# Performance work log

Measured on AMD Instinct MI355X. Metric: run time of the kernel, lower is better.

## Reference

```python
import jax, jax.numpy as jnp
import numpy as np

D_MODEL = 1024
N_HEAD = 16
HEAD_SIZE = D_MODEL // N_HEAD


def setup_inputs() -> dict:
    key = jax.random.key(0)
    ks = jax.random.split(key, 7)
    B, T, E = 2, 2048, D_MODEL
    scale = 0.02
    return {
        "q": jax.random.normal(ks[0], (B, T, E), dtype=jnp.float32),
        "k": jax.random.normal(ks[1], (B, T, E), dtype=jnp.float32),
        "v": jax.random.normal(ks[2], (B, T, E), dtype=jnp.float32),
        "Wq": jax.random.normal(ks[3], (E, E), dtype=jnp.float32) * scale,
        "Wk": jax.random.normal(ks[4], (E, E), dtype=jnp.float32) * scale,
        "Wv": jax.random.normal(ks[5], (E, E), dtype=jnp.float32) * scale,
        "Wo": jax.random.normal(ks[6], (E, E), dtype=jnp.float32) * scale,
    }


def reference(q, k, v, Wq, Wk, Wv, Wo):
    B, T, E = q.shape
    # torch nn.Linear(bias=False): y = x @ W.T
    qh = (q @ Wq.T).reshape(B, T, N_HEAD, HEAD_SIZE).transpose(0, 2, 1, 3)  # [B,H,T,Dh]
    kh = (k @ Wk.T).reshape(B, T, N_HEAD, HEAD_SIZE).transpose(0, 2, 1, 3)
    vh = (v @ Wv.T).reshape(B, T, N_HEAD, HEAD_SIZE).transpose(0, 2, 1, 3)

    scale = 1.0 / jnp.sqrt(jnp.asarray(HEAD_SIZE, dtype=q.dtype))
    wei = jnp.einsum("bhqd,bhkd->bhqk", qh, kh) * scale  # [B,H,T,T]

    # causal mask (tril): positions j > i set to -inf
    causal = jnp.tril(jnp.ones((T, T), dtype=bool))
    wei = jnp.where(causal, wei, jnp.asarray(-jnp.inf, dtype=wei.dtype))

    attn = jax.nn.softmax(wei, axis=-1)
    out = jnp.einsum("bhqk,bhkd->bhqd", attn, vh)  # [B,H,T,Dh]
    out = out.transpose(0, 2, 1, 3).reshape(B, T, E)
    return out @ Wo.T  # dropout p=0.0 -> identity
```

## Files before the change

kernel.cpp:

```cpp
#include <hip/hip_runtime.h>
#include <hip/hip_bf16.h>
#include <cstddef>
#include <cstdint>

#define B_SZ   2
#define T_SEQ  2048
#define E_DIM  1024
#define N_HEAD 16
#define HEAD   64

typedef unsigned short u16;
typedef unsigned int u32;
using frag8 = __attribute__((ext_vector_type(8))) short;
using f32x4 = __attribute__((ext_vector_type(4))) float;

__device__ inline u16 f2bf(float x) {
    __hip_bfloat16 h = __float2bfloat16(x);
    return *reinterpret_cast<u16*>(&h);
}

__device__ inline void gl2lds16(const void* g, void* l) {
    auto gp = reinterpret_cast<const __attribute__((address_space(1))) unsigned int*>(
        reinterpret_cast<uintptr_t>(g));
    auto lp = reinterpret_cast<__attribute__((address_space(3))) unsigned int*>(
        reinterpret_cast<uintptr_t>(l));
    __builtin_amdgcn_global_load_lds(gp, lp, 16, 0, 0);
}

struct CastArgs {
    const float* src[7];
    u16* dst[7];
    int n[7];
    float scale[7];
};

__global__ __launch_bounds__(256) void cast_f32_bf16(CastArgs a) {
    const int t = blockIdx.y;
    const int i0 = (blockIdx.x * 256 + threadIdx.x) * 8;
    if (i0 >= a.n[t]) return;
    const float sc = a.scale[t];
    const float4 f0 = *(const float4*)(a.src[t] + i0);
    const float4 f1 = *(const float4*)(a.src[t] + i0 + 4);
    union { u16 s[8]; uint4 v; } r;
    r.s[0] = f2bf(f0.x * sc); r.s[1] = f2bf(f0.y * sc);
    r.s[2] = f2bf(f0.z * sc); r.s[3] = f2bf(f0.w * sc);
    r.s[4] = f2bf(f1.x * sc); r.s[5] = f2bf(f1.y * sc);
    r.s[6] = f2bf(f1.z * sc); r.s[7] = f2bf(f1.w * sc);
    *(uint4*)(a.dst[t] + i0) = r.v;
}

__device__ inline void gemm_core(const u16* __restrict__ X,
                                 const u16* __restrict__ W,
                                 void* __restrict__ Yv, int mode,
                                 int bm0, int bn0) {
    __shared__ u16 As[2][64 * 64];
    __shared__ u16 Bs[2][128 * 64];

    const int tid = threadIdx.x;
    const int w = tid >> 6;
    const int lane = tid & 63;
    const int ln = lane & 15;
    const int quad = lane >> 4;
    const int wm = (w & 1) * 32;
    const int wn = (w >> 1) * 64;

    const int l8 = lane >> 3;
    const int g = (lane & 7) ^ l8;

    const u16* Ag = X + (size_t)(bm0 + w * 16 + l8) * 1024 + g * 8;
    const u16* Bg = W + (size_t)(bn0 + w * 32 + l8) * 1024 + g * 8;
    const int al = __builtin_amdgcn_readfirstlane(w * 1024);
    const int bl = __builtin_amdgcn_readfirstlane(w * 2048);

    const f32x4 zf = {0.f, 0.f, 0.f, 0.f};
    f32x4 acc[2][4];
#pragma unroll
    for (int mi = 0; mi < 2; ++mi)
#pragma unroll
        for (int nj = 0; nj < 4; ++nj) acc[mi][nj] = zf;

    const int sw = ln & 7;

    gl2lds16(Ag, &As[0][0] + al);
    gl2lds16(Ag + 8 * 1024, &As[0][0] + al + 512);
#pragma unroll
    for (int it = 0; it < 4; ++it)
        gl2lds16(Bg + (size_t)it * 8 * 1024, &Bs[0][0] + bl + it * 512);

    for (int k0 = 0; k0 < 1024; k0 += 64) {
        const int buf = (k0 >> 6) & 1;
        __syncthreads();

        if (k0 + 64 < 1024) {
            gl2lds16(Ag + k0 + 64, &As[buf ^ 1][0] + al);
            gl2lds16(Ag + 8 * 1024 + k0 + 64, &As[buf ^ 1][0] + al + 512);
#pragma unroll
            for (int it = 0; it < 4; ++it)
                gl2lds16(Bg + (size_t)it * 8 * 1024 + k0 + 64,
                         &Bs[buf ^ 1][0] + bl + it * 512);
        }

        frag8 a[2][2], b[4][2];
#pragma unroll
        for (int kc = 0; kc < 2; ++kc) {
            const int slot = ((kc * 4 + quad) ^ sw) * 8;
#pragma unroll
            for (int mi = 0; mi < 2; ++mi)
                a[mi][kc] = *(const frag8*)(&As[buf][0] + (wm + mi * 16 + ln) * 64 + slot);
#pragma unroll
            for (int nj = 0; nj < 4; ++nj)
                b[nj][kc] = *(const frag8*)(&Bs[buf][0] + (wn + nj * 16 + ln) * 64 + slot);
        }
#pragma unroll
        for (int kc = 0; kc < 2; ++kc)
#pragma unroll
            for (int mi = 0; mi < 2; ++mi)
#pragma unroll
                for (int nj = 0; nj < 4; ++nj)
                    acc[mi][nj] = __builtin_amdgcn_mfma_f32_16x16x32_bf16(
                        a[mi][kc], b[nj][kc], acc[mi][nj], 0, 0, 0);
    }

#pragma unroll
    for (int mi = 0; mi < 2; ++mi)
#pragma unroll
        for (int nj = 0; nj < 4; ++nj)
#pragma unroll
            for (int reg = 0; reg < 4; ++reg) {
                const int m = bm0 + wm + mi * 16 + quad * 4 + reg;
                const int n = bn0 + wn + nj * 16 + ln;
                if (mode == 1) {
                    ((float*)Yv)[(size_t)m * E_DIM + n] = acc[mi][nj][reg];
                } else {
                    const int b_ = m >> 11, t_ = m & (T_SEQ - 1);
                    const int h_ = n >> 6, d_ = n & (HEAD - 1);
                    const size_t idx = (mode == 0)
                        ? (((size_t)(b_ * N_HEAD + h_)) * T_SEQ + t_) * HEAD + d_
                        : (((size_t)(b_ * N_HEAD + h_)) * HEAD + d_) * T_SEQ + t_;
                    ((u16*)Yv)[idx] = f2bf(acc[mi][nj][reg]);
                }
            }
}

struct QkvArgs {
    const u16* X[3];
    const u16* W[3];
    u16* Y[3];
};

__global__ __launch_bounds__(256, 3) void gemm_qkv(QkvArgs a) {
    const int z = blockIdx.z;
    gemm_core(a.X[z], a.W[z], a.Y[z], z == 2 ? 2 : 0,
              blockIdx.x * 64, blockIdx.y * 128);
}

__global__ __launch_bounds__(256, 3) void gemm_out(const u16* __restrict__ X,
                                                   const u16* __restrict__ W,
                                                   float* __restrict__ Y) {
    gemm_core(X, W, Y, 1, blockIdx.x * 64, blockIdx.y * 128);
}

__global__ __launch_bounds__(256, 2) void attn_mfma(const u16* __restrict__ Qh,
                                                    const u16* __restrict__ Kh,
                                                    const u16* __restrict__ Vt_g,
                                                    u16* __restrict__ Aa) {
    __shared__ u16 Ks[2][128 * 64];
    __shared__ u16 Vs[2][64 * 128];

    const int tid = threadIdx.x;
    const int w = tid >> 6;
    const int lane = tid & 63;
    const int ln = lane & 15;
    const int quad = lane >> 4;

    const int i = blockIdx.x;
    const int half = i >> 8;
    const int r_ = i & 255;
    const int bh = r_ >> 3;
    const int j = r_ & 7;
    const int qt = half ? j : (15 - j);
    const int q0 = qt * 128;
    const int qw = q0 + w * 32;

    const size_t base = (size_t)bh * T_SEQ * HEAD;
    const u16* Qb = Qh + base;
    const u16* Kb = Kh + base;
    const u16* Vtb = Vt_g + base;

    const int l8 = lane >> 3;
    const int gk = (lane & 7) ^ l8;
    const int l16 = lane >> 4;
    const int c16 = lane & 15;
    const int sls = __builtin_amdgcn_readfirstlane(w * 2048);

    frag8 qf[2][2];
#pragma unroll
    for (int qq = 0; qq < 2; ++qq)
#pragma unroll
        for (int kc = 0; kc < 2; ++kc)
            qf[qq][kc] = *(const frag8*)(Qb + (size_t)(qw + qq * 16 + ln) * HEAD +
                                         kc * 32 + quad * 8);

    const f32x4 zf = {0.f, 0.f, 0.f, 0.f};
    f32x4 o[4][2];
    float rsl[2] = {0.f, 0.f};
#pragma unroll
    for (int dt = 0; dt < 4; ++dt)
#pragma unroll
        for (int qq = 0; qq < 2; ++qq) o[dt][qq] = zf;

    const int ktiles = qt + 1;

#pragma unroll
    for (int it = 0; it < 4; ++it) {
        const int krow = w * 32 + it * 8 + l8;
        gl2lds16(Kb + (size_t)krow * HEAD + gk * 8, &Ks[0][0] + sls + it * 512);
        const int vrow = w * 16 + it * 4 + l16;
        const int gv = c16 ^ (vrow & 7);
        gl2lds16(Vtb + (size_t)vrow * T_SEQ + gv * 8, &Vs[0][0] + sls + it * 512);
    }

    const int sw = ln & 7;
    const int hsel = quad >> 1;
    const int s_lo = ((quad & 1) * 2) * 16 + ln;
    const int s_hi = s_lo + 16;

    for (int kt = 0; kt < ktiles; ++kt) {
        const int k0 = kt << 7;
        const int buf = kt & 1;
        __syncthreads();

        if (kt + 1 < ktiles) {
            const int k1 = k0 + 128;
#pragma unroll
            for (int it = 0; it < 4; ++it) {
                const int krow = w * 32 + it * 8 + l8;
                gl2lds16(Kb + (size_t)(k1 + krow) * HEAD + gk * 8,
                         &Ks[buf ^ 1][0] + sls + it * 512);
                const int vrow = w * 16 + it * 4 + l16;
                const int gv = c16 ^ (vrow & 7);
                gl2lds16(Vtb + (size_t)vrow * T_SEQ + k1 + gv * 8,
                         &Vs[buf ^ 1][0] + sls + it * 512);
            }
        }

        const bool msk = (k0 + 127 > qw);
        u32 pk[8][2][2];
#pragma unroll
        for (int kk = 0; kk < 8; ++kk) {
            f32x4 st[2] = {zf, zf};
#pragma unroll
            for (int kc = 0; kc < 2; ++kc) {
                const int slot = ((kc * 4 + quad) ^ sw) * 8;
                const frag8 kf = *(const frag8*)(&Ks[buf][0] + (kk * 16 + ln) * 64 + slot);
                st[0] = __builtin_amdgcn_mfma_f32_16x16x32_bf16(kf, qf[0][kc], st[0], 0, 0, 0);
                st[1] = __builtin_amdgcn_mfma_f32_16x16x32_bf16(kf, qf[1][kc], st[1], 0, 0, 0);
            }
#pragma unroll
            for (int qq = 0; qq < 2; ++qq) {
                float e[4];
#pragma unroll
                for (int reg = 0; reg < 4; ++reg) {
                    const int key = k0 + kk * 16 + quad * 4 + reg;
                    const int qg = qw + qq * 16 + ln;
                    float ev = __expf(st[qq][reg]);
                    if (msk) ev = (key <= qg) ? ev : 0.f;
                    e[reg] = ev;
                    rsl[qq] += ev;
                }
                pk[kk][qq][0] = ((u32)f2bf(e[1]) << 16) | f2bf(e[0]);
                pk[kk][qq][1] = ((u32)f2bf(e[3]) << 16) | f2bf(e[2]);
            }
        }

#pragma unroll
        for (int kc = 0; kc < 4; ++kc) {
            union { frag8 f; u32 d[4]; } pb[2];
#pragma unroll
            for (int qq = 0; qq < 2; ++qq) {
                const u32 a00 = __shfl(pk[kc * 2][qq][0], s_lo, 64);
                const u32 a01 = __shfl(pk[kc * 2][qq][1], s_lo, 64);
                const u32 a02 = __shfl(pk[kc * 2][qq][0], s_hi, 64);
                const u32 a03 = __shfl(pk[kc * 2][qq][1], s_hi, 64);
                const u32 a10 = __shfl(pk[kc * 2 + 1][qq][0], s_lo, 64);
                const u32 a11 = __shfl(pk[kc * 2 + 1][qq][1], s_lo, 64);
                const u32 a12 = __shfl(pk[kc * 2 + 1][qq][0], s_hi, 64);
                const u32 a13 = __shfl(pk[kc * 2 + 1][qq][1], s_hi, 64);
                pb[qq].d[0] = hsel ? a10 : a00;
                pb[qq].d[1] = hsel ? a11 : a01;
                pb[qq].d[2] = hsel ? a12 : a02;
                pb[qq].d[3] = hsel ? a13 : a03;
            }
            const int slot = ((kc * 4 + quad) ^ sw) * 8;
#pragma unroll
            for (int dt = 0; dt < 4; ++dt) {
                const frag8 vf = *(const frag8*)(&Vs[buf][0] + (dt * 16 + ln) * 128 + slot);
                o[dt][0] = __builtin_amdgcn_mfma_f32_16x16x32_bf16(vf, pb[0].f, o[dt][0], 0, 0, 0);
                o[dt][1] = __builtin_amdgcn_mfma_f32_16x16x32_bf16(vf, pb[1].f, o[dt][1], 0, 0, 0);
            }
        }
    }

#pragma unroll
    for (int qq = 0; qq < 2; ++qq) {
        rsl[qq] += __shfl_xor(rsl[qq], 16, 64);
        rsl[qq] += __shfl_xor(rsl[qq], 32, 64);
    }
    const float inv0 = 1.f / rsl[0];
    const float inv1 = 1.f / rsl[1];
    const int b_ = bh >> 4, h_ = bh & (N_HEAD - 1);
#pragma unroll
    for (int qq = 0; qq < 2; ++qq) {
        const float inv = qq ? inv1 : inv0;
        const int qg = qw + qq * 16 + ln;
        u16* rowp = Aa + ((size_t)(b_ * T_SEQ + qg)) * E_DIM + h_ * HEAD;
#pragma unroll
        for (int dt = 0; dt < 4; ++dt)
#pragma unroll
            for (int rp = 0; rp < 2; ++rp) {
                const u32 v = ((u32)f2bf(o[dt][qq][2 * rp + 1] * inv) << 16) |
                              f2bf(o[dt][qq][2 * rp] * inv);
                *(u32*)(rowp + dt * 16 + quad * 4 + rp * 2) = v;
            }
    }
}

extern "C" void kernel_launch(void* const* d_in, const int* in_sizes, int n_in,
                              void* d_out, int out_size, void* d_ws, size_t ws_size,
                              hipStream_t stream) {
    const float* q  = (const float*)d_in[0];
    const float* k  = (const float*)d_in[1];
    const float* v  = (const float*)d_in[2];
    const float* Wq = (const float*)d_in[3];
    const float* Wk = (const float*)d_in[4];
    const float* Wv = (const float*)d_in[5];
    const float* Wo = (const float*)d_in[6];

    u16* ws = (u16*)d_ws;
    const size_t M4 = (size_t)4 * 1024 * 1024;
    const size_t M1 = (size_t)1024 * 1024;
    u16* qb  = ws;
    u16* kb  = ws + M4;
    u16* vb  = ws + 2 * M4;
    u16* Wqb = ws + 3 * M4;
    u16* Wkb = ws + 3 * M4 + M1;
    u16* Wvb = ws + 3 * M4 + 2 * M1;
    u16* Wob = ws + 3 * M4 + 3 * M1;
    u16* Qh  = ws + 4 * M4;
    u16* Kh  = ws + 5 * M4;
    u16* Vht = ws + 6 * M4;
    u16* Aa  = ws + 7 * M4;

    CastArgs ca;
    ca.src[0] = q;  ca.src[1] = k;  ca.src[2] = v;
    ca.src[3] = Wq; ca.src[4] = Wk; ca.src[5] = Wv; ca.src[6] = Wo;
    ca.dst[0] = qb;  ca.dst[1] = kb;  ca.dst[2] = vb;
    ca.dst[3] = Wqb; ca.dst[4] = Wkb; ca.dst[5] = Wvb; ca.dst[6] = Wob;
    ca.n[0] = ca.n[1] = ca.n[2] = (int)M4;
    ca.n[3] = ca.n[4] = ca.n[5] = ca.n[6] = (int)M1;
    ca.scale[0] = ca.scale[1] = ca.scale[2] = 1.f;
    ca.scale[3] = 0.125f;
    ca.scale[4] = ca.scale[5] = ca.scale[6] = 1.f;
    cast_f32_bf16<<<dim3(2048, 7), 256, 0, stream>>>(ca);

    QkvArgs ga;
    ga.X[0] = qb;  ga.X[1] = kb;  ga.X[2] = vb;
    ga.W[0] = Wqb; ga.W[1] = Wkb; ga.W[2] = Wvb;
    ga.Y[0] = Qh;  ga.Y[1] = Kh;  ga.Y[2] = Vht;
    gemm_qkv<<<dim3(64, 8, 3), 256, 0, stream>>>(ga);

    attn_mfma<<<dim3(512), 256, 0, stream>>>(Qh, Kh, Vht, Aa);

    gemm_out<<<dim3(64, 8), 256, 0, stream>>>(Aa, Wob, (float*)d_out);
}
```

Measured before the change: 207.1 us.

## Split attention key tiles across two wave groups with LDS reduction

Doubles the attention block to 512 threads: the two groups of four waves share the same query rows and each handles half of every 128-key tile. Partial output accumulators and row sums are combined through LDS at the end. Wave groups whose key half lies wholly above the causal diagonal skip their work. This is meant to raise wave parallelism and shorten each wave's serial key loop, at the cost of an extra reduction, more barriers and tighter register limits from launch_bounds(512,4).

```diff
diff --git a/kernel.cpp b/kernel.cpp
--- a/kernel.cpp
+++ b/kernel.cpp
@@ -160,7 +160,7 @@
     gemm_core(X, W, Y, 1, blockIdx.x * 64, blockIdx.y * 128);
 }
 
-__global__ __launch_bounds__(256, 2) void attn_mfma(const u16* __restrict__ Qh,
+__global__ __launch_bounds__(512, 4) void attn_mfma(const u16* __restrict__ Qh,
                                                     const u16* __restrict__ Kh,
                                                     const u16* __restrict__ Vt_g,
                                                     u16* __restrict__ Aa) {
@@ -169,6 +169,8 @@
 
     const int tid = threadIdx.x;
     const int w = tid >> 6;
+    const int wq = w & 3;
+    const int wk = w >> 2;
     const int lane = tid & 63;
     const int ln = lane & 15;
     const int quad = lane >> 4;
@@ -180,7 +182,7 @@
     const int j = r_ & 7;
     const int qt = half ? j : (15 - j);
     const int q0 = qt * 128;
-    const int qw = q0 + w * 32;
+    const int qw = q0 + wq * 32;
 
     const size_t base = (size_t)bh * T_SEQ * HEAD;
     const u16* Qb = Qh + base;
@@ -191,7 +193,7 @@
     const int gk = (lane & 7) ^ l8;
     const int l16 = lane >> 4;
     const int c16 = lane & 15;
-    const int sls = __builtin_amdgcn_readfirstlane(w * 2048);
+    const int sls = __builtin_amdgcn_readfirstlane(w * 1024);
 
     frag8 qf[2][2];
 #pragma unroll
@@ -212,10 +214,10 @@
     const int ktiles = qt + 1;
 
 #pragma unroll
-    for (int it = 0; it < 4; ++it) {
-        const int krow = w * 32 + it * 8 + l8;
+    for (int it = 0; it < 2; ++it) {
+        const int krow = w * 16 + it * 8 + l8;
         gl2lds16(Kb + (size_t)krow * HEAD + gk * 8, &Ks[0][0] + sls + it * 512);
-        const int vrow = w * 16 + it * 4 + l16;
+        const int vrow = w * 8 + it * 4 + l16;
         const int gv = c16 ^ (vrow & 7);
         gl2lds16(Vtb + (size_t)vrow * T_SEQ + gv * 8, &Vs[0][0] + sls + it * 512);
     }
@@ -233,70 +235,74 @@
         if (kt + 1 < ktiles) {
             const int k1 = k0 + 128;
 #pragma unroll
-            for (int it = 0; it < 4; ++it) {
-                const int krow = w * 32 + it * 8 + l8;
+            for (int it = 0; it < 2; ++it) {
+                const int krow = w * 16 + it * 8 + l8;
                 gl2lds16(Kb + (size_t)(k1 + krow) * HEAD + gk * 8,
                          &Ks[buf ^ 1][0] + sls + it * 512);
-                const int vrow = w * 16 + it * 4 + l16;
+                const int vrow = w * 8 + it * 4 + l16;
                 const int gv = c16 ^ (vrow & 7);
                 gl2lds16(Vtb + (size_t)vrow * T_SEQ + k1 + gv * 8,
                          &Vs[buf ^ 1][0] + sls + it * 512);
             }
         }
 
-        const bool msk = (k0 + 127 > qw);
-        u32 pk[8][2][2];
-#pragma unroll
-        for (int kk = 0; kk < 8; ++kk) {
-            f32x4 st[2] = {zf, zf};
+        const int kbase = k0 + wk * 64;
+        if (kbase <= qw + 31) {
+            const bool msk = (kbase + 63 > qw);
+            u32 pk[4][2][2];
+#pragma unroll
+            for (int kk = 0; kk < 4; ++kk) {
+                f32x4 st[2] = {zf, zf};
+#pragma unroll
+                for (int kc = 0; kc < 2; ++kc) {
+                    const int slot = ((kc * 4 + quad) ^ sw) * 8;
+                    const frag8 kf = *(const frag8*)(&Ks[buf][0] +
+                                                     (wk * 64 + kk * 16 + ln) * 64 + slot);
+                    st[0] = __builtin_amdgcn_mfma_f32_16x16x32_bf16(kf, qf[0][kc], st[0], 0, 0, 0);
+                    st[1] = __builtin_amdgcn_mfma_f32_16x16x32_bf16(kf, qf[1][kc], st[1], 0, 0, 0);
+                }
+#pragma unroll
+                for (int qq = 0; qq < 2; ++qq) {
+                    float e[4];
+#pragma unroll
+                    for (int reg = 0; reg < 4; ++reg) {
+                        const int key = kbase + kk * 16 + quad * 4 + reg;
+                        const int qg = qw + qq * 16 + ln;
+                        float ev = __expf(st[qq][reg]);
+                        if (msk) ev = (key <= qg) ? ev : 0.f;
+                        e[reg] = ev;
+                        rsl[qq] += ev;
+                    }
+                    pk[kk][qq][0] = ((u32)f2bf(e[1]) << 16) | f2bf(e[0]);
+                    pk[kk][qq][1] = ((u32)f2bf(e[3]) << 16) | f2bf(e[2]);
+                }
+            }
+
 #pragma unroll
             for (int kc = 0; kc < 2; ++kc) {
-                const int slot = ((kc * 4 + quad) ^ sw) * 8;
-                const frag8 kf = *(const frag8*)(&Ks[buf][0] + (kk * 16 + ln) * 64 + slot);
-                st[0] = __builtin_amdgcn_mfma_f32_16x16x32_bf16(kf, qf[0][kc], st[0], 0, 0, 0);
-                st[1] = __builtin_amdgcn_mfma_f32_16x16x32_bf16(kf, qf[1][kc], st[1], 0, 0, 0);
-            }
-#pragma unroll
-            for (int qq = 0; qq < 2; ++qq) {
-                float e[4];
-#pragma unroll
-                for (int reg = 0; reg < 4; ++reg) {
-                    const int key = k0 + kk * 16 + quad * 4 + reg;
-                    const int qg = qw + qq * 16 + ln;
-                    float ev = __expf(st[qq][reg]);
-                    if (msk) ev = (key <= qg) ? ev : 0.f;
-                    e[reg] = ev;
-                    rsl[qq] += ev;
-                }
-                pk[kk][qq][0] = ((u32)f2bf(e[1]) << 16) | f2bf(e[0]);
-                pk[kk][qq][1] = ((u32)f2bf(e[3]) << 16) | f2bf(e[2]);
-            }
-        }
-
-#pragma unroll
-        for (int kc = 0; kc < 4; ++kc) {
-            union { frag8 f; u32 d[4]; } pb[2];
-#pragma unroll
-            for (int qq = 0; qq < 2; ++qq) {
-                const u32 a00 = __shfl(pk[kc * 2][qq][0], s_lo, 64);
-                const u32 a01 = __shfl(pk[kc * 2][qq][1], s_lo, 64);
-                const u32 a02 = __shfl(pk[kc * 2][qq][0], s_hi, 64);
-                const u32 a03 = __shfl(pk[kc * 2][qq][1], s_hi, 64);
-                const u32 a10 = __shfl(pk[kc * 2 + 1][qq][0], s_lo, 64);
-                const u32 a11 = __shfl(pk[kc * 2 + 1][qq][1], s_lo, 64);
-                const u32 a12 = __shfl(pk[kc * 2 + 1][qq][0], s_hi, 64);
-                const u32 a13 = __shfl(pk[kc * 2 + 1][qq][1], s_hi, 64);
-                pb[qq].d[0] = hsel ? a10 : a00;
-                pb[qq].d[1] = hsel ? a11 : a01;
-                pb[qq].d[2] = hsel ? a12 : a02;
-                pb[qq].d[3] = hsel ? a13 : a03;
-            }
-            const int slot = ((kc * 4 + quad) ^ sw) * 8;
-#pragma unroll
-            for (int dt = 0; dt < 4; ++dt) {
-                const frag8 vf = *(const frag8*)(&Vs[buf][0] + (dt * 16 + ln) * 128 + slot);
-                o[dt][0] = __builtin_amdgcn_mfma_f32_16x16x32_bf16(vf, pb[0].f, o[dt][0], 0, 0, 0);
-                o[dt][1] = __builtin_amdgcn_mfma_f32_16x16x32_bf16(vf, pb[1].f, o[dt][1], 0, 0, 0);
+                union { frag8 f; u32 d[4]; } pb[2];
+#pragma unroll
+                for (int qq = 0; qq < 2; ++qq) {
+                    const u32 a00 = __shfl(pk[kc * 2][qq][0], s_lo, 64);
+                    const u32 a01 = __shfl(pk[kc * 2][qq][1], s_lo, 64);
+                    const u32 a02 = __shfl(pk[kc * 2][qq][0], s_hi, 64);
+                    const u32 a03 = __shfl(pk[kc * 2][qq][1], s_hi, 64);
+                    const u32 a10 = __shfl(pk[kc * 2 + 1][qq][0], s_lo, 64);
+                    const u32 a11 = __shfl(pk[kc * 2 + 1][qq][1], s_lo, 64);
+                    const u32 a12 = __shfl(pk[kc * 2 + 1][qq][0], s_hi, 64);
+                    const u32 a13 = __shfl(pk[kc * 2 + 1][qq][1], s_hi, 64);
+                    pb[qq].d[0] = hsel ? a10 : a00;
+                    pb[qq].d[1] = hsel ? a11 : a01;
+                    pb[qq].d[2] = hsel ? a12 : a02;
+                    pb[qq].d[3] = hsel ? a13 : a03;
+                }
+                const int slotv = (((wk * 2 + kc) * 4 + quad) ^ sw) * 8;
+#pragma unroll
+                for (int dt = 0; dt < 4; ++dt) {
+                    const frag8 vf = *(const frag8*)(&Vs[buf][0] + (dt * 16 + ln) * 128 + slotv);
+                    o[dt][0] = __builtin_amdgcn_mfma_f32_16x16x32_bf16(vf, pb[0].f, o[dt][0], 0, 0, 0);
+                    o[dt][1] = __builtin_amdgcn_mfma_f32_16x16x32_bf16(vf, pb[1].f, o[dt][1], 0, 0, 0);
+                }
             }
         }
     }
@@ -306,22 +312,50 @@
         rsl[qq] += __shfl_xor(rsl[qq], 16, 64);
         rsl[qq] += __shfl_xor(rsl[qq], 32, 64);
     }
-    const float inv0 = 1.f / rsl[0];
-    const float inv1 = 1.f / rsl[1];
-    const int b_ = bh >> 4, h_ = bh & (N_HEAD - 1);
-#pragma unroll
-    for (int qq = 0; qq < 2; ++qq) {
-        const float inv = qq ? inv1 : inv0;
-        const int qg = qw + qq * 16 + ln;
-        u16* rowp = Aa + ((size_t)(b_ * T_SEQ + qg)) * E_DIM + h_ * HEAD;
+
+    __syncthreads();
+    float* ored = (float*)&Ks[0][0];
+    float* lred = (float*)&Vs[0][0];
+    if (wk == 1) {
 #pragma unroll
         for (int dt = 0; dt < 4; ++dt)
 #pragma unroll
-            for (int rp = 0; rp < 2; ++rp) {
-                const u32 v = ((u32)f2bf(o[dt][qq][2 * rp + 1] * inv) << 16) |
-                              f2bf(o[dt][qq][2 * rp] * inv);
-                *(u32*)(rowp + dt * 16 + quad * 4 + rp * 2) = v;
-            }
+            for (int qq = 0; qq < 2; ++qq)
+#pragma unroll
+                for (int rg = 0; rg < 4; ++rg)
+                    ored[(dt * 8 + qq * 4 + rg) * 256 + wq * 64 + lane] = o[dt][qq][rg];
+        lred[wq * 64 + lane] = rsl[0];
+        lred[256 + wq * 64 + lane] = rsl[1];
+    }
+    __syncthreads();
+    if (wk == 0) {
+#pragma unroll
+        for (int dt = 0; dt < 4; ++dt)
+#pragma unroll
+            for (int qq = 0; qq < 2; ++qq)
+#pragma unroll
+                for (int rg = 0; rg < 4; ++rg)
+                    o[dt][qq][rg] += ored[(dt * 8 + qq * 4 + rg) * 256 + wq * 64 + lane];
+        rsl[0] += lred[wq * 64 + lane];
+        rsl[1] += lred[256 + wq * 64 + lane];
+
+        const float inv0 = 1.f / rsl[0];
+        const float inv1 = 1.f / rsl[1];
+        const int b_ = bh >> 4, h_ = bh & (N_HEAD - 1);
+#pragma unroll
+        for (int qq = 0; qq < 2; ++qq) {
+            const float inv = qq ? inv1 : inv0;
+            const int qg = qw + qq * 16 + ln;
+            u16* rowp = Aa + ((size_t)(b_ * T_SEQ + qg)) * E_DIM + h_ * HEAD;
+#pragma unroll
+            for (int dt = 0; dt < 4; ++dt)
+#pragma unroll
+                for (int rp = 0; rp < 2; ++rp) {
+                    const u32 v = ((u32)f2bf(o[dt][qq][2 * rp + 1] * inv) << 16) |
+                                  f2bf(o[dt][qq][2 * rp] * inv);
+                    *(u32*)(rowp + dt * 16 + quad * 4 + rp * 2) = v;
+                }
+        }
     }
 }
 
@@ -369,7 +403,7 @@
     ga.Y[0] = Qh;  ga.Y[1] = Kh;  ga.Y[2] = Vht;
     gemm_qkv<<<dim3(64, 8, 3), 256, 0, stream>>>(ga);
 
-    attn_mfma<<<dim3(512), 256, 0, stream>>>(Qh, Kh, Vht, Aa);
+    attn_mfma<<<dim3(512), 512, 0, stream>>>(Qh, Kh, Vht, Aa);
 
     gemm_out<<<dim3(64, 8), 256, 0, stream>>>(Aa, Wob, (float*)d_out);
 }
```

Result: faster. 198.6 us (-4.1%).
